# Kernel tuning notes

Hardware: AMD Instinct MI355X
Metric: run time of the kernel (lower is better)

## Reference

```python
import jax, jax.numpy as jnp
import numpy as np

EPS = 0.001
CTX = 8
POWERS = 2.0 ** jnp.arange(CTX - 1, -1, -1, dtype=jnp.float32)  # [2^7,...,1]


def _normalize_rows(x):
    return x / jnp.linalg.norm(x, axis=1, keepdims=True)


def _layer(side, inp, normal, offset, W, bias):
    # inp: None for first layer, else previous layer output
    if inp is None:
        inp = jnp.concatenate([bias, jax.nn.sigmoid(jnp.clip(side, EPS, 1.0 - EPS))])
    else:
        inp = jnp.concatenate([bias, inp])
    bits = (side @ normal > offset).astype(jnp.float32)          # [CTX]
    gating = jnp.dot(bits, POWERS).astype(jnp.int32)              # scalar context index
    logit_in = jnp.log(inp) - jnp.log1p(-inp)                     # torch.logit
    out = jax.nn.sigmoid(logit_in @ W[gating])                    # gather slice + GEMV
    return jnp.clip(out, EPS, 1.0 - EPS)


def setup_inputs() -> dict:
    key = jax.random.key(0)
    ks = jax.random.split(key, 10)
    input_dim, dims = 1024, [1024, 1024, 512, 1]  # [in] + layer_dims + [out]
    side_info = jax.random.normal(ks[0], (input_dim,), dtype=jnp.float32)
    d = {"side_info": side_info}
    for i, (p, c) in enumerate(zip(dims[:-1], dims[1:])):
        d[f"W{i}"] = jnp.full((2 ** CTX, p + 1, c), 1.0 / (p + 1), dtype=jnp.float32)
        d[f"N{i}"] = _normalize_rows(jax.random.normal(ks[1 + i], (input_dim, CTX), dtype=jnp.float32))
        d[f"O{i}"] = jax.random.normal(ks[4 + i], (CTX,), dtype=jnp.float32)
        d[f"B{i}"] = EPS + jax.random.uniform(ks[7 + i], (1,), dtype=jnp.float32) * (1.0 - 2.0 * EPS)
    return d


def reference(side_info, W0, W1, W2, N0, N1, N2, O0, O1, O2, B0, B1, B2):
    side = side_info.astype(jnp.float32)
    out = None
    for W, N, O, B in ((W0, N0, O0, B0), (W1, N1, O1, B1), (W2, N2, O2, B2)):
        out = _layer(side, out, N, O, W, B)
    return out
```

## Files before the change

kernel.cpp:

```cpp
#include <hip/hip_runtime.h>
#include <hip/hip_cooperative_groups.h>
#include <math.h>

namespace cg = cooperative_groups;

#define GLN_EPS 0.001f
#define NBLK 256

__device__ __forceinline__ float clipf_(float v) {
    return fminf(fmaxf(v, GLN_EPS), 1.0f - GLN_EPS);
}
__device__ __forceinline__ float logitf_(float p) {
    return logf(p) - log1pf(-p);
}
__device__ __forceinline__ float sigclip_logit(float z) {
    float s = 1.0f / (1.0f + expf(-z));
    s = clipf_(s);
    return logf(s) - log1pf(-s);
}

struct GlnArgs {
    const float *side, *W0, *N0, *O0, *B0;
    const float *W1, *N1, *O1, *B1;
    const float *W2, *N2, *O2, *B2;
    float* ws;
    float* out;
};


__global__ __launch_bounds__(256) void gln_fused(GlnArgs a)
{
    __shared__ float sred[16 * 64];
    __shared__ float red8[4][8];

    const int bid = blockIdx.x, tid = threadIdx.x;
    float* ws = a.ws;

    if (bid < 3) {
        const float* __restrict__ N = (bid == 0) ? a.N0 : (bid == 1) ? a.N1 : a.N2;
        const float* __restrict__ O = (bid == 0) ? a.O0 : (bid == 1) ? a.O1 : a.O2;
        float p[8];
#pragma unroll
        for (int k = 0; k < 8; ++k) p[k] = 0.0f;
        for (int i = tid; i < 1024; i += 256) {
            const float s = a.side[i];
            const float4* n4 = reinterpret_cast<const float4*>(N + (size_t)i * 8);
            const float4 u = n4[0], v = n4[1];
            p[0] += s * u.x; p[1] += s * u.y; p[2] += s * u.z; p[3] += s * u.w;
            p[4] += s * v.x; p[5] += s * v.y; p[6] += s * v.z; p[7] += s * v.w;
        }
        const int lane = tid & 63, wid = tid >> 6;
#pragma unroll
        for (int k = 0; k < 8; ++k) {
            float v = p[k];
#pragma unroll
            for (int off = 32; off > 0; off >>= 1) v += __shfl_down(v, off);
            if (lane == 0) red8[wid][k] = v;
        }
        __syncthreads();
        if (tid == 0) {
            int g = 0;
#pragma unroll
            for (int k = 0; k < 8; ++k) {
                const float d = red8[0][k] + red8[1][k] + red8[2][k] + red8[3][k];
                if (d > O[k]) g |= 1 << (7 - k);
            }
            reinterpret_cast<int*>(ws)[1536 + bid] = g;
        }
    } else if (bid == 3) {
        for (int i = tid; i < 1536; i += 256) ws[i] = 0.0f;
    }
    cg::this_grid().sync();

    {
        const int g0 = reinterpret_cast<const int*>(ws)[1536];
        const float lb = logitf_(a.B0[0]);
        const size_t base = (size_t)g0 * (1025u * 1024u);
        const int colchunk = bid & 15;
        const int c16 = tid & 15, r16 = tid >> 4;
        const int rowid = ((bid >> 4) << 4) | r16;
        const int col = colchunk * 64 + c16 * 4;

        float4 acc = make_float4(0.f, 0.f, 0.f, 0.f);
        for (int i = rowid; i < 1025; i += 256) {
            const float xi = (i == 0) ? lb : clipf_(a.side[i - 1]);
            const float4 w = *reinterpret_cast<const float4*>(a.W0 + base + (size_t)i * 1024u + col);
            acc.x += xi * w.x; acc.y += xi * w.y; acc.z += xi * w.z; acc.w += xi * w.w;
        }
        *reinterpret_cast<float4*>(&sred[r16 * 64 + c16 * 4]) = acc;
        __syncthreads();
        if (tid < 64) {
            float s = 0.0f;
#pragma unroll
            for (int r = 0; r < 16; ++r) s += sred[r * 64 + tid];
            atomicAdd(&ws[colchunk * 64 + tid], s);
        }
    }
    cg::this_grid().sync();

    {
        const int g1 = reinterpret_cast<const int*>(ws)[1537];
        const float lb = logitf_(a.B1[0]);
        const size_t base = (size_t)g1 * (1025u * 512u);
        const int colchunk = bid & 7;
        const int c16 = tid & 15, r16 = tid >> 4;
        const int rowid = ((bid >> 3) << 4) | r16;
        const int col = colchunk * 64 + c16 * 4;

        float4 acc = make_float4(0.f, 0.f, 0.f, 0.f);
        for (int i = rowid; i < 1025; i += 512) {
            const float xi = (i == 0) ? lb : sigclip_logit(ws[i - 1]);
            const float4 w = *reinterpret_cast<const float4*>(a.W1 + base + (size_t)i * 512u + col);
            acc.x += xi * w.x; acc.y += xi * w.y; acc.z += xi * w.z; acc.w += xi * w.w;
        }
        __syncthreads();
        *reinterpret_cast<float4*>(&sred[r16 * 64 + c16 * 4]) = acc;
        __syncthreads();
        if (tid < 64) {
            float s = 0.0f;
#pragma unroll
            for (int r = 0; r < 16; ++r) s += sred[r * 64 + tid];
            atomicAdd(&ws[1024 + colchunk * 64 + tid], s);
        }
    }
    cg::this_grid().sync();

    if (bid == 0) {
        const int g2 = reinterpret_cast<const int*>(ws)[1538];
        const float lb = logitf_(a.B2[0]);
        const size_t base = (size_t)g2 * 513u;
        float partial = 0.0f;
        for (int i = tid; i < 513; i += 256) {
            const float xi = (i == 0) ? lb : sigclip_logit(ws[1024 + i - 1]);
            partial += xi * a.W2[base + i];
        }
#pragma unroll
        for (int off = 32; off > 0; off >>= 1) partial += __shfl_down(partial, off);
        __syncthreads();
        if ((tid & 63) == 0) red8[tid >> 6][0] = partial;
        __syncthreads();
        if (tid == 0) {
            const float z = red8[0][0] + red8[1][0] + red8[2][0] + red8[3][0];
            a.out[0] = clipf_(1.0f / (1.0f + expf(-z)));
        }
    }
}

extern "C" void kernel_launch(void* const* d_in, const int* in_sizes, int n_in,
                              void* d_out, int out_size, void* d_ws, size_t ws_size,
                              hipStream_t stream) {
    GlnArgs a;
    a.side = (const float*)d_in[0];
    a.W0 = (const float*)d_in[1];  a.N0 = (const float*)d_in[2];
    a.O0 = (const float*)d_in[3];  a.B0 = (const float*)d_in[4];
    a.W1 = (const float*)d_in[5];  a.N1 = (const float*)d_in[6];
    a.O1 = (const float*)d_in[7];  a.B1 = (const float*)d_in[8];
    a.W2 = (const float*)d_in[9];  a.N2 = (const float*)d_in[10];
    a.O2 = (const float*)d_in[11]; a.B2 = (const float*)d_in[12];
    a.ws  = (float*)d_ws;
    a.out = (float*)d_out;

    void* params[] = { &a };
    hipLaunchCooperativeKernel(reinterpret_cast<void*>(gln_fused),
                               dim3(NBLK), dim3(256), params, 0, stream);
}
```

Baseline: 1.500 ms.

## Replace cooperative grid syncs with three regular launches and last-block finalize

Splits the single cooperative kernel into three ordinary launches (prep, layer-0 GEMV, layer-1 GEMV plus final layer), so stream ordering replaces the first two grid-wide barriers. The last grid barrier becomes a threadfence plus an atomic counter, and whichever block finishes last computes the final dot product. This removes the cooperative-launch overhead and the cost of the grid sync, at the price of two extra kernel launch latencies.

Result: faster. 1.365 ms (-9.0%).

```diff
diff --git a/kernel.cpp b/kernel.cpp
--- a/kernel.cpp
+++ b/kernel.cpp
@@ -1,11 +1,7 @@
 #include <hip/hip_runtime.h>
-#include <hip/hip_cooperative_groups.h>
 #include <math.h>
 
-namespace cg = cooperative_groups;
-
 #define GLN_EPS 0.001f
-#define NBLK 256
 
 __device__ __forceinline__ float clipf_(float v) {
     return fminf(fmaxf(v, GLN_EPS), 1.0f - GLN_EPS);
@@ -19,148 +15,176 @@
     return logf(s) - log1pf(-s);
 }
 
-struct GlnArgs {
-    const float *side, *W0, *N0, *O0, *B0;
-    const float *W1, *N1, *O1, *B1;
-    const float *W2, *N2, *O2, *B2;
-    float* ws;
-    float* out;
-};
 
+__global__ __launch_bounds__(256) void gln_prep(
+    const float* __restrict__ side,
+    const float* __restrict__ N0, const float* __restrict__ O0,
+    const float* __restrict__ N1, const float* __restrict__ O1,
+    const float* __restrict__ N2, const float* __restrict__ O2,
+    float* __restrict__ ws)
+{
+    const int bid = blockIdx.x, tid = threadIdx.x;
+    if (bid == 3) {
+        for (int i = tid; i < 1536; i += 256) ws[i] = 0.0f;
+        if (tid == 0) reinterpret_cast<int*>(ws)[1540] = 0;
+        return;
+    }
+    const float* __restrict__ N = (bid == 0) ? N0 : (bid == 1) ? N1 : N2;
+    const float* __restrict__ O = (bid == 0) ? O0 : (bid == 1) ? O1 : O2;
 
-__global__ __launch_bounds__(256) void gln_fused(GlnArgs a)
+    float p[8];
+#pragma unroll
+    for (int k = 0; k < 8; ++k) p[k] = 0.0f;
+    for (int i = tid; i < 1024; i += 256) {
+        const float s = side[i];
+        const float4* n4 = reinterpret_cast<const float4*>(N + (size_t)i * 8);
+        const float4 u = n4[0], v = n4[1];
+        p[0] += s * u.x; p[1] += s * u.y; p[2] += s * u.z; p[3] += s * u.w;
+        p[4] += s * v.x; p[5] += s * v.y; p[6] += s * v.z; p[7] += s * v.w;
+    }
+    __shared__ float red8[4][8];
+    const int lane = tid & 63, wid = tid >> 6;
+#pragma unroll
+    for (int k = 0; k < 8; ++k) {
+        float v = p[k];
+#pragma unroll
+        for (int off = 32; off > 0; off >>= 1) v += __shfl_down(v, off);
+        if (lane == 0) red8[wid][k] = v;
+    }
+    __syncthreads();
+    if (tid == 0) {
+        int g = 0;
+#pragma unroll
+        for (int k = 0; k < 8; ++k) {
+            const float d = red8[0][k] + red8[1][k] + red8[2][k] + red8[3][k];
+            if (d > O[k]) g |= 1 << (7 - k);
+        }
+        reinterpret_cast<int*>(ws)[1536 + bid] = g;
+    }
+}
+
+__global__ __launch_bounds__(256) void gln_gemv0(
+    const float* __restrict__ side,
+    const float* __restrict__ W0,
+    const float* __restrict__ B0,
+    float* __restrict__ ws)
 {
     __shared__ float sred[16 * 64];
-    __shared__ float red8[4][8];
+    const int bid = blockIdx.x, tid = threadIdx.x;
+    const int g0 = reinterpret_cast<const int*>(ws)[1536];
+    const float lb = logitf_(B0[0]);
+    const size_t base = (size_t)g0 * (1025u * 1024u);
+    const int colchunk = bid & 15;
+    const int c16 = tid & 15, r16 = tid >> 4;
+    const int rowid = ((bid >> 4) << 4) | r16;
+    const int col = colchunk * 64 + c16 * 4;
 
+    float4 acc = make_float4(0.f, 0.f, 0.f, 0.f);
+    for (int i = rowid; i < 1025; i += 256) {
+        const float xi = (i == 0) ? lb : clipf_(side[i - 1]);
+        const float4 w = *reinterpret_cast<const float4*>(W0 + base + (size_t)i * 1024u + col);
+        acc.x += xi * w.x; acc.y += xi * w.y; acc.z += xi * w.z; acc.w += xi * w.w;
+    }
+    *reinterpret_cast<float4*>(&sred[r16 * 64 + c16 * 4]) = acc;
+    __syncthreads();
+    if (tid < 64) {
+        float s = 0.0f;
+#pragma unroll
+        for (int r = 0; r < 16; ++r) s += sred[r * 64 + tid];
+        atomicAdd(&ws[colchunk * 64 + tid], s);
+    }
+}
+
+__global__ __launch_bounds__(256) void gln_gemv1_final(
+    const float* __restrict__ W1,
+    const float* __restrict__ B1,
+    const float* __restrict__ W2,
+    const float* __restrict__ B2,
+    float* __restrict__ ws,
+    float* __restrict__ out)
+{
+    __shared__ float sred[16 * 64];
+    __shared__ int is_last_s;
     const int bid = blockIdx.x, tid = threadIdx.x;
-    float* ws = a.ws;
+    const int g1 = reinterpret_cast<const int*>(ws)[1537];
+    const float lb = logitf_(B1[0]);
+    const size_t base = (size_t)g1 * (1025u * 512u);
+    const int colchunk = bid & 7;
+    const int c16 = tid & 15, r16 = tid >> 4;
+    const int rowid = ((bid >> 3) << 4) | r16;
+    const int col = colchunk * 64 + c16 * 4;
 
-    if (bid < 3) {
-        const float* __restrict__ N = (bid == 0) ? a.N0 : (bid == 1) ? a.N1 : a.N2;
-        const float* __restrict__ O = (bid == 0) ? a.O0 : (bid == 1) ? a.O1 : a.O2;
-        float p[8];
+    float4 acc = make_float4(0.f, 0.f, 0.f, 0.f);
+    for (int i = rowid; i < 1025; i += 512) {
+        const float xi = (i == 0) ? lb : sigclip_logit(ws[i - 1]);
+        const float4 w = *reinterpret_cast<const float4*>(W1 + base + (size_t)i * 512u + col);
+        acc.x += xi * w.x; acc.y += xi * w.y; acc.z += xi * w.z; acc.w += xi * w.w;
+    }
+    *reinterpret_cast<float4*>(&sred[r16 * 64 + c16 * 4]) = acc;
+    __syncthreads();
+    if (tid < 64) {
+        float s = 0.0f;
 #pragma unroll
-        for (int k = 0; k < 8; ++k) p[k] = 0.0f;
-        for (int i = tid; i < 1024; i += 256) {
-            const float s = a.side[i];
-            const float4* n4 = reinterpret_cast<const float4*>(N + (size_t)i * 8);
-            const float4 u = n4[0], v = n4[1];
-            p[0] += s * u.x; p[1] += s * u.y; p[2] += s * u.z; p[3] += s * u.w;
-            p[4] += s * v.x; p[5] += s * v.y; p[6] += s * v.z; p[7] += s * v.w;
+        for (int r = 0; r < 16; ++r) s += sred[r * 64 + tid];
+        atomicAdd(&ws[1024 + colchunk * 64 + tid], s);
+    }
+
+    __threadfence();
+    if (tid == 0) {
+        const int old = atomicAdd(&reinterpret_cast<int*>(ws)[1540], 1);
+        is_last_s = (old == (int)gridDim.x - 1);
+    }
+    __syncthreads();
+    if (!is_last_s) return;
+    __threadfence();
+
+    const int g2 = reinterpret_cast<const int*>(ws)[1538];
+    const size_t b2 = (size_t)g2 * 513u;
+    const float lb2 = logitf_(B2[0]);
+    float partial = 0.0f;
+    for (int i = tid; i < 513; i += 256) {
+        float xi;
+        if (i == 0) xi = lb2;
+        else {
+            const float z = __hip_atomic_load(&ws[1024 + i - 1], __ATOMIC_RELAXED,
+                                              __HIP_MEMORY_SCOPE_AGENT);
+            xi = sigclip_logit(z);
         }
-        const int lane = tid & 63, wid = tid >> 6;
+        partial += xi * W2[b2 + i];
+    }
 #pragma unroll
-        for (int k = 0; k < 8; ++k) {
-            float v = p[k];
-#pragma unroll
-            for (int off = 32; off > 0; off >>= 1) v += __shfl_down(v, off);
-            if (lane == 0) red8[wid][k] = v;
-        }
-        __syncthreads();
-        if (tid == 0) {
-            int g = 0;
-#pragma unroll
-            for (int k = 0; k < 8; ++k) {
-                const float d = red8[0][k] + red8[1][k] + red8[2][k] + red8[3][k];
-                if (d > O[k]) g |= 1 << (7 - k);
-            }
-            reinterpret_cast<int*>(ws)[1536 + bid] = g;
-        }
-    } else if (bid == 3) {
-        for (int i = tid; i < 1536; i += 256) ws[i] = 0.0f;
-    }
-    cg::this_grid().sync();
-
-    {
-        const int g0 = reinterpret_cast<const int*>(ws)[1536];
-        const float lb = logitf_(a.B0[0]);
-        const size_t base = (size_t)g0 * (1025u * 1024u);
-        const int colchunk = bid & 15;
-        const int c16 = tid & 15, r16 = tid >> 4;
-        const int rowid = ((bid >> 4) << 4) | r16;
-        const int col = colchunk * 64 + c16 * 4;
-
-        float4 acc = make_float4(0.f, 0.f, 0.f, 0.f);
-        for (int i = rowid; i < 1025; i += 256) {
-            const float xi = (i == 0) ? lb : clipf_(a.side[i - 1]);
-            const float4 w = *reinterpret_cast<const float4*>(a.W0 + base + (size_t)i * 1024u + col);
-            acc.x += xi * w.x; acc.y += xi * w.y; acc.z += xi * w.z; acc.w += xi * w.w;
-        }
-        *reinterpret_cast<float4*>(&sred[r16 * 64 + c16 * 4]) = acc;
-        __syncthreads();
-        if (tid < 64) {
-            float s = 0.0f;
-#pragma unroll
-            for (int r = 0; r < 16; ++r) s += sred[r * 64 + tid];
-            atomicAdd(&ws[colchunk * 64 + tid], s);
-        }
-    }
-    cg::this_grid().sync();
-
-    {
-        const int g1 = reinterpret_cast<const int*>(ws)[1537];
-        const float lb = logitf_(a.B1[0]);
-        const size_t base = (size_t)g1 * (1025u * 512u);
-        const int colchunk = bid & 7;
-        const int c16 = tid & 15, r16 = tid >> 4;
-        const int rowid = ((bid >> 3) << 4) | r16;
-        const int col = colchunk * 64 + c16 * 4;
-
-        float4 acc = make_float4(0.f, 0.f, 0.f, 0.f);
-        for (int i = rowid; i < 1025; i += 512) {
-            const float xi = (i == 0) ? lb : sigclip_logit(ws[i - 1]);
-            const float4 w = *reinterpret_cast<const float4*>(a.W1 + base + (size_t)i * 512u + col);
-            acc.x += xi * w.x; acc.y += xi * w.y; acc.z += xi * w.z; acc.w += xi * w.w;
-        }
-        __syncthreads();
-        *reinterpret_cast<float4*>(&sred[r16 * 64 + c16 * 4]) = acc;
-        __syncthreads();
-        if (tid < 64) {
-            float s = 0.0f;
-#pragma unroll
-            for (int r = 0; r < 16; ++r) s += sred[r * 64 + tid];
-            atomicAdd(&ws[1024 + colchunk * 64 + tid], s);
-        }
-    }
-    cg::this_grid().sync();
-
-    if (bid == 0) {
-        const int g2 = reinterpret_cast<const int*>(ws)[1538];
-        const float lb = logitf_(a.B2[0]);
-        const size_t base = (size_t)g2 * 513u;
-        float partial = 0.0f;
-        for (int i = tid; i < 513; i += 256) {
-            const float xi = (i == 0) ? lb : sigclip_logit(ws[1024 + i - 1]);
-            partial += xi * a.W2[base + i];
-        }
-#pragma unroll
-        for (int off = 32; off > 0; off >>= 1) partial += __shfl_down(partial, off);
-        __syncthreads();
-        if ((tid & 63) == 0) red8[tid >> 6][0] = partial;
-        __syncthreads();
-        if (tid == 0) {
-            const float z = red8[0][0] + red8[1][0] + red8[2][0] + red8[3][0];
-            a.out[0] = clipf_(1.0f / (1.0f + expf(-z)));
-        }
+    for (int off = 32; off > 0; off >>= 1) partial += __shfl_down(partial, off);
+    __syncthreads();
+    if ((tid & 63) == 0) sred[tid >> 6] = partial;
+    __syncthreads();
+    if (tid == 0) {
+        const float z = sred[0] + sred[1] + sred[2] + sred[3];
+        out[0] = clipf_(1.0f / (1.0f + expf(-z)));
     }
 }
 
 extern "C" void kernel_launch(void* const* d_in, const int* in_sizes, int n_in,
                               void* d_out, int out_size, void* d_ws, size_t ws_size,
                               hipStream_t stream) {
-    GlnArgs a;
-    a.side = (const float*)d_in[0];
-    a.W0 = (const float*)d_in[1];  a.N0 = (const float*)d_in[2];
-    a.O0 = (const float*)d_in[3];  a.B0 = (const float*)d_in[4];
-    a.W1 = (const float*)d_in[5];  a.N1 = (const float*)d_in[6];
-    a.O1 = (const float*)d_in[7];  a.B1 = (const float*)d_in[8];
-    a.W2 = (const float*)d_in[9];  a.N2 = (const float*)d_in[10];
-    a.O2 = (const float*)d_in[11]; a.B2 = (const float*)d_in[12];
-    a.ws  = (float*)d_ws;
-    a.out = (float*)d_out;
+    const float* side = (const float*)d_in[0];
+    const float* W0   = (const float*)d_in[1];
+    const float* N0   = (const float*)d_in[2];
+    const float* O0   = (const float*)d_in[3];
+    const float* B0   = (const float*)d_in[4];
+    const float* W1   = (const float*)d_in[5];
+    const float* N1   = (const float*)d_in[6];
+    const float* O1   = (const float*)d_in[7];
+    const float* B1   = (const float*)d_in[8];
+    const float* W2   = (const float*)d_in[9];
+    const float* N2   = (const float*)d_in[10];
+    const float* O2   = (const float*)d_in[11];
+    const float* B2   = (const float*)d_in[12];
+    float* out = (float*)d_out;
+    float* ws  = (float*)d_ws;
 
-    void* params[] = { &a };
-    hipLaunchCooperativeKernel(reinterpret_cast<void*>(gln_fused),
-                               dim3(NBLK), dim3(256), params, 0, stream);
+    hipLaunchKernelGGL(gln_prep,        dim3(4),   dim3(256), 0, stream,
+                       side, N0, O0, N1, O1, N2, O2, ws);
+    hipLaunchKernelGGL(gln_gemv0,       dim3(256), dim3(256), 0, stream, side, W0, B0, ws);
+    hipLaunchKernelGGL(gln_gemv1_final, dim3(256), dim3(256), 0, stream,
+                       W1, B1, W2, B2, ws, out);
 }
```
